# Kernel optimization log

Measured on AMD Instinct MI355X. Metric: run time of the kernel, lower is better.

## Reference

```python
import jax, jax.numpy as jnp
import numpy as np

GMIN, GMAX = 0.1, 1.0
DIMS = [3, 256, 256, 256, 1]

def setup_inputs() -> dict:
    key = jax.random.key(0)
    ks = jax.random.split(key, 12)
    inp = {"pos": jax.random.normal(ks[0], (1048576, 3), dtype=jnp.float32)}
    for i in range(4):
        fan_in = DIMS[i]
        bound = 1.0 / np.sqrt(fan_in)
        inp[f"W{i}"] = jax.random.uniform(ks[1 + 2 * i], (fan_in, DIMS[i + 1]), jnp.float32, -bound, bound)
        inp[f"b{i}"] = jax.random.uniform(ks[2 + 2 * i], (DIMS[i + 1],), jnp.float32, -bound, bound)
    for i in range(3):
        inp[f"sigma{i}"] = jax.random.uniform(ks[9 + i], (256,), jnp.float32, GMIN, GMAX)
    return inp

def _gauss(x, sigma):
    # Gaussian activation: exp(-x^2 / (2*sigma^2)), sigma learnable per-feature
    return jnp.exp(-jnp.square(x) / (2.0 * jnp.square(sigma)))

def _softplus8(x):
    # torch Softplus(beta=1, threshold=8): linear beyond threshold
    return jnp.where(x > 8.0, x, jnp.log1p(jnp.exp(jnp.minimum(x, 8.0))))

def reference(pos, W0, b0, W1, b1, W2, b2, W3, b3, sigma0, sigma1, sigma2):
    h = _gauss(pos @ W0 + b0, sigma0)      # [N,256]
    h = _gauss(h @ W1 + b1, sigma1)        # [N,256]
    h = _gauss(h @ W2 + b2, sigma2)        # [N,256]
    return _softplus8(h @ W3 + b3)         # [N,1]
```

## Files before the change

### kernel.cpp

```cpp
#include <hip/hip_runtime.h>
#include <hip/hip_bf16.h>
#include <math.h>

typedef __attribute__((ext_vector_type(8))) short short8;
typedef __attribute__((ext_vector_type(4))) float f32x4;
typedef __attribute__((ext_vector_type(2))) float f32x2;
typedef __attribute__((ext_vector_type(2))) unsigned int uint2v;

#define LOG2E 1.4426950408889634f
#define LN2   0.6931471805599453f

__device__ __forceinline__ unsigned short f2bf(float f) {
    union { float f; unsigned u; } v; v.f = f;
    unsigned u = v.u;
    u += 0x7fffu + ((u >> 16) & 1u);
    return (unsigned short)(u >> 16);
}
__device__ __forceinline__ float bf2f(unsigned short h) {
    union { unsigned u; float f; } v; v.u = ((unsigned)h) << 16;
    return v.f;
}
__device__ __forceinline__ unsigned pk_bf16(float a, float b) {
    __hip_bfloat162 t = __float22bfloat162_rn(float2{a, b});
    union { __hip_bfloat162 b; unsigned u; } v; v.b = t;
    return v.u;
}
__device__ __forceinline__ f32x2 pk_add2(f32x2 a, f32x2 b) {
    f32x2 d;
    asm("v_pk_add_f32 %0, %1, %2" : "=v"(d) : "v"(a), "v"(b));
    return d;
}
__device__ __forceinline__ f32x2 pk_mul2(f32x2 a, f32x2 b) {
    f32x2 d;
    asm("v_pk_mul_f32 %0, %1, %2" : "=v"(d) : "v"(a), "v"(b));
    return d;
}

__global__ void pack_kernel(const float* __restrict__ W0, const float* __restrict__ W1,
                            const float* __restrict__ W2, const float* __restrict__ W3,
                            const float* __restrict__ s0, const float* __restrict__ s1,
                            const float* __restrict__ s2,
                            const float* __restrict__ b0, const float* __restrict__ b1,
                            const float* __restrict__ b2,
                            unsigned short* __restrict__ wp, float* __restrict__ negc) {
    int tid = blockIdx.x * 256 + threadIdx.x;
    if (tid < 8192) {
        int j = tid & 7, lane = (tid >> 3) & 63, ct = (tid >> 9) & 3, w = tid >> 11;
        int k = ((lane >> 4) * 8) + j;
        int n = w * 64 + 4 * (lane & 15) + ct;
        unsigned short v = 0;
        if (k < 9) {
            int d = k / 3, m = k - d * 3;
            float sv = s0[n];
            float sc = sqrtf(LOG2E / (2.0f * sv * sv));
            float wv = W0[d * 256 + n] * sc;
            unsigned short wh = f2bf(wv);
            v = (m == 1) ? f2bf(wv - bf2f(wh)) : wh;
        }
        wp[tid] = v;
    } else if (tid < 139264) {
        int e = tid - 8192;
        const float* W = W1;
        const float* S = s1;
        if (e >= 65536) { W = W2; S = s2; e -= 65536; }
        int j = e & 7, lane = (e >> 3) & 63, ct = (e >> 9) & 3, ks = (e >> 11) & 7, w = e >> 14;
        int k = ks * 32 + ((lane >> 4) * 8) + j;
        int n = w * 64 + 4 * (lane & 15) + ct;
        float sv = S[n];
        float sc = sqrtf(LOG2E / (2.0f * sv * sv));
        wp[tid] = f2bf(W[k * 256 + n] * sc);
    } else if (tid < 143360) {
        int e = tid - 139264;
        int j = e & 7, lane = (e >> 3) & 63, ks = (e >> 9) & 1, w = e >> 10;
        int i16p = lane & 15, qp = lane >> 4;
        int k = w * 64 + ks * 32 + qp * 8 + j;
        float wv = W3[k];
        unsigned short wh = f2bf(wv);
        unsigned short v = 0;
        if (i16p == 0) v = wh;
        else if (i16p == 1) v = f2bf(wv - bf2f(wh));
        wp[139264 + e] = v;
    }
    if (tid < 768) {
        int l = tid >> 8, n = tid & 255;
        const float* s = (l == 0) ? s0 : (l == 1 ? s1 : s2);
        const float* b = (l == 0) ? b0 : (l == 1 ? b1 : b2);
        float sv = s[n], bv = b[n];
        float sc = sqrtf(LOG2E / (2.0f * sv * sv));
        negc[l * 256 + n] = sc * bv;
    }
}

constexpr int ROWS = 64;
constexpr int HSTR = 264;
constexpr int ASTR = 40;

template <int NKS, int SSTR>
__device__ __forceinline__ void layer(const unsigned short* __restrict__ src,
                                      const unsigned short* __restrict__ wpk,
                                      const float* __restrict__ ncp,
                                      unsigned short* __restrict__ hdst,
                                      int w, int i16, int q, bool presync) {
    f32x4 acc[4][4];
#pragma unroll
    for (int rg = 0; rg < 4; ++rg)
#pragma unroll
        for (int ct = 0; ct < 4; ++ct)
            acc[rg][ct] = f32x4{0.f, 0.f, 0.f, 0.f};

    const int lane = q * 16 + i16;
    const short8* wp8 = (const short8*)wpk + (w * NKS * 4) * 64 + lane;
    const unsigned short* abase = src + i16 * SSTR + q * 8;

#pragma unroll
    for (int ks = 0; ks < NKS; ++ks) {
        short8 a[4];
#pragma unroll
        for (int rg = 0; rg < 4; ++rg)
            a[rg] = *(const short8*)(abase + rg * 16 * SSTR + ks * 32);
#pragma unroll
        for (int ct = 0; ct < 4; ++ct) {
            short8 wf = wp8[(ks * 4 + ct) * 64];
#pragma unroll
            for (int rg = 0; rg < 4; ++rg)
                acc[rg][ct] = __builtin_amdgcn_mfma_f32_16x16x32_bf16(a[rg], wf, acc[rg][ct], 0, 0, 0);
        }
    }

    const int ce = w * 64 + 4 * i16;
    const f32x4 T = *(const f32x4*)(ncp + ce);
    f32x2 tb[4];
#pragma unroll
    for (int ct = 0; ct < 4; ++ct) tb[ct] = f32x2{T[ct], T[ct]};
    uint2v av[4][4];
#pragma unroll
    for (int rg = 0; rg < 4; ++rg) {
        float gg[4][4];
#pragma unroll
        for (int ct = 0; ct < 4; ++ct) {
            f32x2 xlo = f32x2{acc[rg][ct][0], acc[rg][ct][1]};
            f32x2 xhi = f32x2{acc[rg][ct][2], acc[rg][ct][3]};
            f32x2 ylo = pk_add2(xlo, tb[ct]);
            f32x2 yhi = pk_add2(xhi, tb[ct]);
            f32x2 wlo = pk_mul2(ylo, ylo);
            f32x2 whi = pk_mul2(yhi, yhi);
            gg[0][ct] = __builtin_amdgcn_exp2f(-wlo[0]);
            gg[1][ct] = __builtin_amdgcn_exp2f(-wlo[1]);
            gg[2][ct] = __builtin_amdgcn_exp2f(-whi[0]);
            gg[3][ct] = __builtin_amdgcn_exp2f(-whi[1]);
        }
#pragma unroll
        for (int rr = 0; rr < 4; ++rr) {
            uint2v v;
            v[0] = pk_bf16(gg[rr][0], gg[rr][1]);
            v[1] = pk_bf16(gg[rr][2], gg[rr][3]);
            av[rg][rr] = v;
        }
    }
    if (presync) __syncthreads();
#pragma unroll
    for (int rg = 0; rg < 4; ++rg) {
        int rbase = rg * 16 + q * 4;
#pragma unroll
        for (int rr = 0; rr < 4; ++rr)
            *(uint2v*)&hdst[(rbase + rr) * HSTR + ce] = av[rg][rr];
    }
    __syncthreads();
}

__global__ __launch_bounds__(256, 4) void mlp_kernel(
    const float* __restrict__ pos,
    const float* __restrict__ b3,
    const unsigned short* __restrict__ Wp,
    const float* __restrict__ negc,
    float* __restrict__ out)
{
    __shared__ unsigned short h[ROWS * HSTR];
    __shared__ unsigned short A0[ROWS * ASTR];

    const int tid  = threadIdx.x;
    const int lane = tid & 63;
    const int wave = tid >> 6;
    const int i16  = lane & 15, q = lane >> 4;
    const long row0 = (long)blockIdx.x * ROWS;

    if (tid < ROWS) {
        const float* pp = pos + (row0 + tid) * 3;
        float p0 = pp[0], p1 = pp[1], p2 = pp[2];
        short h0 = (short)f2bf(p0); short l0 = (short)f2bf(p0 - bf2f((unsigned short)h0));
        short h1 = (short)f2bf(p1); short l1 = (short)f2bf(p1 - bf2f((unsigned short)h1));
        short h2 = (short)f2bf(p2); short l2 = (short)f2bf(p2 - bf2f((unsigned short)h2));
        unsigned short* arow = A0 + tid * ASTR;
        *(short8*)(arow + 0)  = short8{h0, h0, l0, h1, h1, l1, h2, h2};
        *(short8*)(arow + 8)  = short8{l2, 0, 0, 0, 0, 0, 0, 0};
        *(short8*)(arow + 16) = short8{0, 0, 0, 0, 0, 0, 0, 0};
        *(short8*)(arow + 24) = short8{0, 0, 0, 0, 0, 0, 0, 0};
    }
    __syncthreads();

    layer<1, ASTR>(A0, Wp,         negc,        h, wave, i16, q, false);
    layer<8, HSTR>(h,  Wp + 8192,  negc + 256,  h, wave, i16, q, true);
    layer<8, HSTR>(h,  Wp + 73728, negc + 512,  h, wave, i16, q, true);

    {
        const short8* w3p = (const short8*)(Wp + 139264) + (wave * 2) * 64 + lane;
        const unsigned short* ab3 = h + i16 * HSTR + wave * 64 + q * 8;
        f32x4 acc3[4];
#pragma unroll
        for (int rg = 0; rg < 4; ++rg) acc3[rg] = f32x4{0.f, 0.f, 0.f, 0.f};
#pragma unroll
        for (int ks = 0; ks < 2; ++ks) {
            short8 wf = w3p[ks * 64];
#pragma unroll
            for (int rg = 0; rg < 4; ++rg) {
                short8 a = *(const short8*)(ab3 + rg * 16 * HSTR + ks * 32);
                acc3[rg] = __builtin_amdgcn_mfma_f32_16x16x32_bf16(a, wf, acc3[rg], 0, 0, 0);
            }
        }
        float* scr = (float*)A0;
        if (i16 < 2) {
#pragma unroll
            for (int rg = 0; rg < 4; ++rg)
                *(f32x4*)&scr[(wave * 2 + i16) * 64 + rg * 16 + q * 4] = acc3[rg];
        }
        __syncthreads();
        if (tid < 64) {
            float s = 0.f;
#pragma unroll
            for (int g = 0; g < 8; ++g) s += scr[g * 64 + tid];
            float x  = s + b3[0];
            float xm = fminf(x, 8.0f);
            float e  = __builtin_amdgcn_exp2f(xm * LOG2E);
            float sp = __builtin_amdgcn_logf(1.0f + e) * LN2;
            out[row0 + tid] = (x > 8.0f) ? x : sp;
        }
    }
}

extern "C" void kernel_launch(void* const* d_in, const int* in_sizes, int n_in,
                              void* d_out, int out_size, void* d_ws, size_t ws_size,
                              hipStream_t stream) {
    const float* pos = (const float*)d_in[0];
    const float* W0  = (const float*)d_in[1];
    const float* b0  = (const float*)d_in[2];
    const float* W1  = (const float*)d_in[3];
    const float* b1  = (const float*)d_in[4];
    const float* W2  = (const float*)d_in[5];
    const float* b2  = (const float*)d_in[6];
    const float* W3  = (const float*)d_in[7];
    const float* b3  = (const float*)d_in[8];
    const float* s0  = (const float*)d_in[9];
    const float* s1  = (const float*)d_in[10];
    const float* s2  = (const float*)d_in[11];

    unsigned short* wp = (unsigned short*)d_ws;
    float* negc = (float*)((char*)d_ws + 286720);

    pack_kernel<<<560, 256, 0, stream>>>(W0, W1, W2, W3, s0, s1, s2, b0, b1, b2, wp, negc);

    int nrows = in_sizes[0] / 3;
    int nblk  = nrows / ROWS;
    mlp_kernel<<<nblk, 256, 0, stream>>>(pos, b3, wp, negc,
                                         (float*)d_out);
}
```

Measured before the change: 376.4 us.

## Ping-pong two 64-row halves across eight waves to overlap MFMA with activations

Each block now holds 128 rows split into two 64-row halves with separate LDS buffers, and runs 512 threads (eight waves), each owning 32 output columns. The layers are interleaved so that one half's Gaussian activation and bf16 store run alongside the other half's matrix multiply, hiding exp and LDS-write latency behind MFMA work. The weight packing is rearranged to match the 32-column-per-wave split. In exchange, LDS use per block roughly doubles, which may limit how many blocks fit on a CU, and each wave gets less MFMA work per A-fragment load.

```diff
diff --git a/kernel.cpp b/kernel.cpp
--- a/kernel.cpp
+++ b/kernel.cpp
@@ -5,7 +5,6 @@
 typedef __attribute__((ext_vector_type(8))) short short8;
 typedef __attribute__((ext_vector_type(4))) float f32x4;
 typedef __attribute__((ext_vector_type(2))) float f32x2;
-typedef __attribute__((ext_vector_type(2))) unsigned int uint2v;
 
 #define LOG2E 1.4426950408889634f
 #define LN2   0.6931471805599453f
@@ -45,9 +44,9 @@
                             unsigned short* __restrict__ wp, float* __restrict__ negc) {
     int tid = blockIdx.x * 256 + threadIdx.x;
     if (tid < 8192) {
-        int j = tid & 7, lane = (tid >> 3) & 63, ct = (tid >> 9) & 3, w = tid >> 11;
+        int j = tid & 7, lane = (tid >> 3) & 63, ct = (tid >> 9) & 1, w = (tid >> 10) & 7;
         int k = ((lane >> 4) * 8) + j;
-        int n = w * 64 + 4 * (lane & 15) + ct;
+        int n = w * 32 + 2 * (lane & 15) + ct;
         unsigned short v = 0;
         if (k < 9) {
             int d = k / 3, m = k - d * 3;
@@ -63,17 +62,17 @@
         const float* W = W1;
         const float* S = s1;
         if (e >= 65536) { W = W2; S = s2; e -= 65536; }
-        int j = e & 7, lane = (e >> 3) & 63, ct = (e >> 9) & 3, ks = (e >> 11) & 7, w = e >> 14;
+        int j = e & 7, lane = (e >> 3) & 63, ct = (e >> 9) & 1, ks = (e >> 10) & 7, w = (e >> 13) & 7;
         int k = ks * 32 + ((lane >> 4) * 8) + j;
-        int n = w * 64 + 4 * (lane & 15) + ct;
+        int n = w * 32 + 2 * (lane & 15) + ct;
         float sv = S[n];
         float sc = sqrtf(LOG2E / (2.0f * sv * sv));
         wp[tid] = f2bf(W[k * 256 + n] * sc);
     } else if (tid < 143360) {
         int e = tid - 139264;
-        int j = e & 7, lane = (e >> 3) & 63, ks = (e >> 9) & 1, w = e >> 10;
+        int j = e & 7, lane = (e >> 3) & 63, w = (e >> 9) & 7;
         int i16p = lane & 15, qp = lane >> 4;
-        int k = w * 64 + ks * 32 + qp * 8 + j;
+        int k = w * 32 + qp * 8 + j;
         float wv = W3[k];
         unsigned short wh = f2bf(wv);
         unsigned short v = 0;
@@ -91,27 +90,20 @@
     }
 }
 
-constexpr int ROWS = 64;
+constexpr int ROWS = 128;
 constexpr int HSTR = 264;
 constexpr int ASTR = 40;
 
 template <int NKS, int SSTR>
-__device__ __forceinline__ void layer(const unsigned short* __restrict__ src,
-                                      const unsigned short* __restrict__ wpk,
-                                      const float* __restrict__ ncp,
-                                      unsigned short* __restrict__ hdst,
-                                      int w, int i16, int q, bool presync) {
-    f32x4 acc[4][4];
+__device__ __forceinline__ void mfma_tile(const unsigned short* __restrict__ src,
+                                          const short8* __restrict__ wp8,
+                                          f32x4 (&acc)[4][2], int i16, int q) {
 #pragma unroll
     for (int rg = 0; rg < 4; ++rg)
 #pragma unroll
-        for (int ct = 0; ct < 4; ++ct)
+        for (int ct = 0; ct < 2; ++ct)
             acc[rg][ct] = f32x4{0.f, 0.f, 0.f, 0.f};
-
-    const int lane = q * 16 + i16;
-    const short8* wp8 = (const short8*)wpk + (w * NKS * 4) * 64 + lane;
     const unsigned short* abase = src + i16 * SSTR + q * 8;
-
 #pragma unroll
     for (int ks = 0; ks < NKS; ++ks) {
         short8 a[4];
@@ -119,69 +111,57 @@
         for (int rg = 0; rg < 4; ++rg)
             a[rg] = *(const short8*)(abase + rg * 16 * SSTR + ks * 32);
 #pragma unroll
-        for (int ct = 0; ct < 4; ++ct) {
-            short8 wf = wp8[(ks * 4 + ct) * 64];
+        for (int ct = 0; ct < 2; ++ct) {
+            short8 wf = wp8[(ks * 2 + ct) * 64];
 #pragma unroll
             for (int rg = 0; rg < 4; ++rg)
                 acc[rg][ct] = __builtin_amdgcn_mfma_f32_16x16x32_bf16(a[rg], wf, acc[rg][ct], 0, 0, 0);
         }
     }
-
-    const int ce = w * 64 + 4 * i16;
-    const f32x4 T = *(const f32x4*)(ncp + ce);
-    f32x2 tb[4];
-#pragma unroll
-    for (int ct = 0; ct < 4; ++ct) tb[ct] = f32x2{T[ct], T[ct]};
-    uint2v av[4][4];
+}
+
+__device__ __forceinline__ void act_store(f32x4 (&acc)[4][2],
+                                          const float* __restrict__ ncp,
+                                          unsigned short* __restrict__ hdst,
+                                          int cbase, int q) {
+    const f32x2 T = *(const f32x2*)(ncp + cbase);
 #pragma unroll
     for (int rg = 0; rg < 4; ++rg) {
-        float gg[4][4];
-#pragma unroll
-        for (int ct = 0; ct < 4; ++ct) {
-            f32x2 xlo = f32x2{acc[rg][ct][0], acc[rg][ct][1]};
-            f32x2 xhi = f32x2{acc[rg][ct][2], acc[rg][ct][3]};
-            f32x2 ylo = pk_add2(xlo, tb[ct]);
-            f32x2 yhi = pk_add2(xhi, tb[ct]);
+        float g[4][2];
+#pragma unroll
+        for (int ct = 0; ct < 2; ++ct) {
+            f32x2 tb = f32x2{T[ct], T[ct]};
+            f32x2 ylo = pk_add2(f32x2{acc[rg][ct][0], acc[rg][ct][1]}, tb);
+            f32x2 yhi = pk_add2(f32x2{acc[rg][ct][2], acc[rg][ct][3]}, tb);
             f32x2 wlo = pk_mul2(ylo, ylo);
             f32x2 whi = pk_mul2(yhi, yhi);
-            gg[0][ct] = __builtin_amdgcn_exp2f(-wlo[0]);
-            gg[1][ct] = __builtin_amdgcn_exp2f(-wlo[1]);
-            gg[2][ct] = __builtin_amdgcn_exp2f(-whi[0]);
-            gg[3][ct] = __builtin_amdgcn_exp2f(-whi[1]);
-        }
-#pragma unroll
-        for (int rr = 0; rr < 4; ++rr) {
-            uint2v v;
-            v[0] = pk_bf16(gg[rr][0], gg[rr][1]);
-            v[1] = pk_bf16(gg[rr][2], gg[rr][3]);
-            av[rg][rr] = v;
-        }
-    }
-    if (presync) __syncthreads();
-#pragma unroll
-    for (int rg = 0; rg < 4; ++rg) {
-        int rbase = rg * 16 + q * 4;
+            g[0][ct] = __builtin_amdgcn_exp2f(-wlo[0]);
+            g[1][ct] = __builtin_amdgcn_exp2f(-wlo[1]);
+            g[2][ct] = __builtin_amdgcn_exp2f(-whi[0]);
+            g[3][ct] = __builtin_amdgcn_exp2f(-whi[1]);
+        }
 #pragma unroll
         for (int rr = 0; rr < 4; ++rr)
-            *(uint2v*)&hdst[(rbase + rr) * HSTR + ce] = av[rg][rr];
-    }
-    __syncthreads();
-}
-
-__global__ __launch_bounds__(256, 4) void mlp_kernel(
+            *(unsigned*)&hdst[(rg * 16 + q * 4 + rr) * HSTR + cbase] = pk_bf16(g[rr][0], g[rr][1]);
+    }
+}
+
+__global__ __launch_bounds__(512, 4) void mlp_kernel(
     const float* __restrict__ pos,
     const float* __restrict__ b3,
     const unsigned short* __restrict__ Wp,
     const float* __restrict__ negc,
     float* __restrict__ out)
 {
-    __shared__ unsigned short h[ROWS * HSTR];
+    __shared__ unsigned short hA[64 * HSTR];
+    __shared__ unsigned short hB[64 * HSTR];
     __shared__ unsigned short A0[ROWS * ASTR];
 
     const int tid  = threadIdx.x;
     const int lane = tid & 63;
-    const int wave = tid >> 6;
+    const int w    = tid >> 6;
     const int i16  = lane & 15, q = lane >> 4;
+    const int cbase = w * 32 + 2 * i16;
     const long row0 = (long)blockIdx.x * ROWS;
 
     if (tid < ROWS) {
@@ -198,42 +178,83 @@
     }
     __syncthreads();
 
-    layer<1, ASTR>(A0, Wp,         negc,        h, wave, i16, q, false);
-    layer<8, HSTR>(h,  Wp + 8192,  negc + 256,  h, wave, i16, q, true);
-    layer<8, HSTR>(h,  Wp + 73728, negc + 512,  h, wave, i16, q, true);
+    f32x4 accA[4][2], accB[4][2];
+    const short8* wp0 = (const short8*)Wp + (w * 2) * 64 + lane;
+    const short8* wp1 = (const short8*)(Wp + 8192)  + (w * 16) * 64 + lane;
+    const short8* wp2 = (const short8*)(Wp + 73728) + (w * 16) * 64 + lane;
+
+    mfma_tile<1, ASTR>(A0,             wp0, accA, i16, q);
+    mfma_tile<1, ASTR>(A0 + 64 * ASTR, wp0, accB, i16, q);
+    act_store(accA, negc, hA, cbase, q);
+    __syncthreads();
+    mfma_tile<8, HSTR>(hA, wp1, accA, i16, q);
+    act_store(accB, negc, hB, cbase, q);
+    __syncthreads();
+    mfma_tile<8, HSTR>(hB, wp1, accB, i16, q);
+    act_store(accA, negc + 256, hA, cbase, q);
+    __syncthreads();
+    mfma_tile<8, HSTR>(hA, wp2, accA, i16, q);
+    act_store(accB, negc + 256, hB, cbase, q);
+    __syncthreads();
+    mfma_tile<8, HSTR>(hB, wp2, accB, i16, q);
+    act_store(accA, negc + 512, hA, cbase, q);
+    __syncthreads();
+
+    const short8* w3p = (const short8*)(Wp + 139264) + w * 64 + lane;
+    short8 wf3 = w3p[0];
+    float* scrA = (float*)A0;
+    float* scrB = scrA + 1024;
+    f32x4 acc3A[4], acc3B[4];
 
     {
-        const short8* w3p = (const short8*)(Wp + 139264) + (wave * 2) * 64 + lane;
-        const unsigned short* ab3 = h + i16 * HSTR + wave * 64 + q * 8;
-        f32x4 acc3[4];
-#pragma unroll
-        for (int rg = 0; rg < 4; ++rg) acc3[rg] = f32x4{0.f, 0.f, 0.f, 0.f};
-#pragma unroll
-        for (int ks = 0; ks < 2; ++ks) {
-            short8 wf = w3p[ks * 64];
-#pragma unroll
-            for (int rg = 0; rg < 4; ++rg) {
-                short8 a = *(const short8*)(ab3 + rg * 16 * HSTR + ks * 32);
-                acc3[rg] = __builtin_amdgcn_mfma_f32_16x16x32_bf16(a, wf, acc3[rg], 0, 0, 0);
-            }
-        }
-        float* scr = (float*)A0;
-        if (i16 < 2) {
-#pragma unroll
-            for (int rg = 0; rg < 4; ++rg)
-                *(f32x4*)&scr[(wave * 2 + i16) * 64 + rg * 16 + q * 4] = acc3[rg];
-        }
-        __syncthreads();
-        if (tid < 64) {
-            float s = 0.f;
-#pragma unroll
-            for (int g = 0; g < 8; ++g) s += scr[g * 64 + tid];
-            float x  = s + b3[0];
-            float xm = fminf(x, 8.0f);
-            float e  = __builtin_amdgcn_exp2f(xm * LOG2E);
-            float sp = __builtin_amdgcn_logf(1.0f + e) * LN2;
-            out[row0 + tid] = (x > 8.0f) ? x : sp;
-        }
+        const unsigned short* ab3 = hA + i16 * HSTR + w * 32 + q * 8;
+#pragma unroll
+        for (int rg = 0; rg < 4; ++rg) {
+            short8 a = *(const short8*)(ab3 + rg * 16 * HSTR);
+            acc3A[rg] = __builtin_amdgcn_mfma_f32_16x16x32_bf16(a, wf3, f32x4{0.f,0.f,0.f,0.f}, 0, 0, 0);
+        }
+    }
+    act_store(accB, negc + 512, hB, cbase, q);
+    __syncthreads();
+    {
+        const unsigned short* ab3 = hB + i16 * HSTR + w * 32 + q * 8;
+#pragma unroll
+        for (int rg = 0; rg < 4; ++rg) {
+            short8 a = *(const short8*)(ab3 + rg * 16 * HSTR);
+            acc3B[rg] = __builtin_amdgcn_mfma_f32_16x16x32_bf16(a, wf3, f32x4{0.f,0.f,0.f,0.f}, 0, 0, 0);
+        }
+    }
+    if (i16 < 2) {
+#pragma unroll
+        for (int rg = 0; rg < 4; ++rg)
+            *(f32x4*)&scrA[(w * 2 + i16) * 64 + rg * 16 + q * 4] = acc3A[rg];
+    }
+    __syncthreads();
+    if (i16 < 2) {
+#pragma unroll
+        for (int rg = 0; rg < 4; ++rg)
+            *(f32x4*)&scrB[(w * 2 + i16) * 64 + rg * 16 + q * 4] = acc3B[rg];
+    }
+    if (tid < 64) {
+        float s = 0.f;
+#pragma unroll
+        for (int g = 0; g < 16; ++g) s += scrA[g * 64 + tid];
+        float x  = s + b3[0];
+        float xm = fminf(x, 8.0f);
+        float e  = __builtin_amdgcn_exp2f(xm * LOG2E);
+        float sp = __builtin_amdgcn_logf(1.0f + e) * LN2;
+        out[row0 + tid] = (x > 8.0f) ? x : sp;
+    }
+    __syncthreads();
+    if (tid < 64) {
+        float s = 0.f;
+#pragma unroll
+        for (int g = 0; g < 16; ++g) s += scrB[g * 64 + tid];
+        float x  = s + b3[0];
+        float xm = fminf(x, 8.0f);
+        float e  = __builtin_amdgcn_exp2f(xm * LOG2E);
+        float sp = __builtin_amdgcn_logf(1.0f + e) * LN2;
+        out[row0 + 64 + tid] = (x > 8.0f) ? x : sp;
     }
 }
 
@@ -260,6 +281,6 @@
 
     int nrows = in_sizes[0] / 3;
     int nblk  = nrows / ROWS;
-    mlp_kernel<<<nblk, 256, 0, stream>>>(pos, b3, wp, negc,
+    mlp_kernel<<<nblk, 512, 0, stream>>>(pos, b3, wp, negc,
                                          (float*)d_out);
 }
```

Result: slower. 494.2 us (+31.3%).
